# Kernel tuning notes

Measured on AMD Instinct MI355X. Metric: run time of the kernel, lower is better.

## Reference

```python
import jax, jax.numpy as jnp
import numpy as np

V, E, H, M = 256, 512, 512, 128
D = 2 * H  # decoder hidden
B, L_TXT, T_MEL = 32, 256, 800
EPS = 1e-5


def setup_inputs() -> dict:
    key = jax.random.key(0)
    ks = jax.random.split(key, 24)
    s = 0.02
    inp = {
        'x': jax.random.randint(ks[0], (B, L_TXT), 0, V),
        'text_seq_lens': jax.random.randint(ks[1], (B,), 1, L_TXT + 1),
        'y': jax.random.normal(ks[2], (B, T_MEL, M), jnp.float32),
        'mel_spec_lens': jax.random.randint(ks[3], (B,), 1, T_MEL + 1),
        'emb': jax.random.normal(ks[4], (V, E)) * s,
        'conv1_w': jax.random.normal(ks[5], (E, E, 3)) * s,
        'conv1_b': jnp.zeros((E,)),
        'bn1_g': jnp.ones((E,)), 'bn1_b': jnp.zeros((E,)),
        'conv2_w': jax.random.normal(ks[6], (E, E, 3)) * s,
        'conv2_b': jnp.zeros((E,)),
        'bn2_g': jnp.ones((E,)), 'bn2_b': jnp.zeros((E,)),
        'wih_f': jax.random.normal(ks[7], (4 * H, E)) * s,
        'whh_f': jax.random.normal(ks[8], (4 * H, H)) * s,
        'bih_f': jnp.zeros((4 * H,)), 'bhh_f': jnp.zeros((4 * H,)),
        'wih_b': jax.random.normal(ks[9], (4 * H, E)) * s,
        'whh_b': jax.random.normal(ks[10], (4 * H, H)) * s,
        'bih_b': jnp.zeros((4 * H,)), 'bhh_b': jnp.zeros((4 * H,)),
        'dwih': jax.random.normal(ks[11], (4 * D, M)) * s,
        'dwhh': jax.random.normal(ks[12], (4 * D, D)) * s,
        'dbih': jnp.zeros((4 * D,)), 'dbhh': jnp.zeros((4 * D,)),
        'proj_w': jax.random.normal(ks[13], (M, D)) * s,
        'proj_b': jnp.zeros((M,)),
        'gate_w': jax.random.normal(ks[14], (1, D)) * s,
        'gate_b': jnp.zeros((1,)),
    }
    return inp


def _conv_bn_relu(x, w, b, g, beta):
    # x: (B, E, L); training-mode BatchNorm (batch statistics, biased var)
    x = jax.lax.conv_general_dilated(x, w, (1,), [(1, 1)],
                                     dimension_numbers=('NCH', 'OIH', 'NCH')) + b[None, :, None]
    mu = jnp.mean(x, axis=(0, 2), keepdims=True)
    var = jnp.mean((x - mu) ** 2, axis=(0, 2), keepdims=True)
    x = (x - mu) * jax.lax.rsqrt(var + EPS) * g[None, :, None] + beta[None, :, None]
    return jax.nn.relu(x)


def _lstm_last(xseq, lens, wih, whh, bih, bhh):
    # Run LSTM over full padded seq, freezing state past each length.
    # Returns final (h, c) == state at t = len-1 (packed-sequence semantics).
    Bb, T, _ = xseq.shape
    Hh = whh.shape[1]
    pre = jnp.einsum('bte,ge->btg', xseq, wih) + bih + bhh  # (B,T,4H)

    def step(carry, inp):
        h, c = carry
        xt, t = inp
        gates = xt + h @ whh.T
        i, f, g, o = jnp.split(gates, 4, axis=-1)
        c_n = jax.nn.sigmoid(f) * c + jax.nn.sigmoid(i) * jnp.tanh(g)
        h_n = jax.nn.sigmoid(o) * jnp.tanh(c_n)
        valid = (t < lens)[:, None]
        return (jnp.where(valid, h_n, h), jnp.where(valid, c_n, c)), None

    init = (jnp.zeros((Bb, Hh), xseq.dtype), jnp.zeros((Bb, Hh), xseq.dtype))
    (h, c), _ = jax.lax.scan(step, init, (pre.transpose(1, 0, 2), jnp.arange(T)))
    return h, c


def _forward(x, text_seq_lens, y, mel_spec_lens, emb, conv1_w, conv1_b, bn1_g, bn1_b,
             conv2_w, conv2_b, bn2_g, bn2_b, wih_f, whh_f, bih_f, bhh_f,
             wih_b, whh_b, bih_b, bhh_b, dwih, dwhh, dbih, dbhh,
             proj_w, proj_b, gate_w, gate_b):
    xe = emb[x]                       # (B, L, E)
    h = xe.transpose(0, 2, 1)         # (B, E, L)
    h = _conv_bn_relu(h, conv1_w, conv1_b, bn1_g, bn1_b)  # dropout = identity (eval)
    h = _conv_bn_relu(h, conv2_w, conv2_b, bn2_g, bn2_b)
    h = h.transpose(0, 2, 1)          # (B, L, E)

    # bidirectional encoder LSTM final states (packed semantics)
    hf, cf = _lstm_last(h, text_seq_lens, wih_f, whh_f, bih_f, bhh_f)
    # reverse each sequence within its valid length for the backward direction
    t_idx = jnp.arange(h.shape[1])[None, :]
    rev_idx = jnp.clip(text_seq_lens[:, None] - 1 - t_idx, 0, h.shape[1] - 1)
    h_rev = jnp.take_along_axis(h, rev_idx[:, :, None], axis=1)
    hb, cb = _lstm_last(h_rev, text_seq_lens, wih_b, whh_b, bih_b, bhh_b)

    hid = jnp.concatenate([hf, hb], axis=1)  # (B, 2H)
    cel = jnp.concatenate([cf, cb], axis=1)

    Tm = y.shape[1]

    def dec_step(carry, _):
        hd, cd, inp = carry
        gates = inp @ dwih.T + dbih + dbhh + hd @ dwhh.T
        i, f, g, o = jnp.split(gates, 4, axis=-1)
        cd = jax.nn.sigmoid(f) * cd + jax.nn.sigmoid(i) * jnp.tanh(g)
        hd = jax.nn.sigmoid(o) * jnp.tanh(cd)
        mel = hd @ proj_w.T + proj_b          # (B, M)
        gate = hd @ gate_w.T + gate_b         # (B, 1)
        return (hd, cd, mel), (mel, gate[:, 0])

    sos = jnp.zeros((y.shape[0], M), y.dtype)
    _, (mels, gates) = jax.lax.scan(dec_step, (hid, cel, sos), None, length=Tm)
    mel_outputs = mels.transpose(1, 0, 2)     # (B, Tm, M)
    gate_outputs = gates.T                    # (B, Tm)

    mask = jnp.arange(Tm)[None, :] > mel_spec_lens[:, None]  # (B, Tm), strictly >
    masked_mel = jnp.where(mask[:, :, None], 0.0, mel_outputs)
    masked_gate = jnp.where(mask, 1000.0, gate_outputs)
    return masked_mel, masked_gate, mask


def reference(x, text_seq_lens, y, mel_spec_lens, emb, conv1_w, conv1_b, bn1_g, bn1_b,
              conv2_w, conv2_b, bn2_g, bn2_b, wih_f, whh_f, bih_f, bhh_f,
              wih_b, whh_b, bih_b, bhh_b, dwih, dwhh, dbih, dbhh,
              proj_w, proj_b, gate_w, gate_b):
    return _forward(x, text_seq_lens, y, mel_spec_lens, emb, conv1_w, conv1_b,
                    bn1_g, bn1_b, conv2_w, conv2_b, bn2_g, bn2_b,
                    wih_f, whh_f, bih_f, bhh_f, wih_b, whh_b, bih_b, bhh_b,
                    dwih, dwhh, dbih, dbhh, proj_w, proj_b, gate_w, gate_b)
```

## Files before the change

### kernel.cpp

```cpp
#include <hip/hip_runtime.h>


typedef float f4 __attribute__((ext_vector_type(4)));
typedef _Float16 h8 __attribute__((ext_vector_type(8)));
typedef _Float16 half_t;
typedef unsigned long long u64;

#define B_    32
#define LTXT  256
#define TMEL  800
#define EE    512
#define HH    512
#define DD    1024
#define MM    128
#define NROWS 8192
#define GATE_OFF 3276800
#define MASK_OFF 3302400

#define RING_D 801
#define RING_E 257
#define HOP    13

#define WS_MBE        0ull
#define WS_MBD        16384ull
#define WS_HENC       49152ull
#define WS_ZERO_BYTES 81920ull
#define WS_HD         16891904ull
#define WS_BUFX       69386240ull
#define WS_BUFY       77774848ull
#define WS_CONVF      86163456ull
#define WS_WEFF       86163456ull
#define WS_W0         94552064ull
#define WS_WP1        102940672ull
#define WS_WP2        104513536ull
#define WS_WIHP       106086400ull
#define WS_WHHP       110280704ull
#define WS_BSUM       114475008ull
#define WS_BEFF       114491392ull
#define WS_B0         114507776ull
#define WS_MEAN       114524160ull
#define WS_RSTD       114526208ull
#define WS_PROJW      114528256ull
#define WS_PROJG      114790400ull
#define WS_CEL        114823168ull

__device__ __forceinline__ float sigm(float x) { return 1.f / (1.f + __expf(-x)); }
__device__ __forceinline__ float tanh_f(float x) {
    float e = __expf(2.f * x);
    return 1.f - 2.f / (e + 1.f);
}

__device__ __forceinline__ void st_atom64(void* p, u64 v) {
    asm volatile("global_atomic_swap_x2 %0, %1, off" :: "v"(p), "v"(v) : "memory");
}
__device__ __forceinline__ void st_atom32(unsigned* p, unsigned v) {
    asm volatile("global_atomic_swap %0, %1, off" :: "v"(p), "v"(v) : "memory");
}


__global__ void k_embed(const int* __restrict__ x, const float* __restrict__ emb,
                        half_t* __restrict__ out) {
    int row = blockIdx.x;
    int tok = x[row];
    const float* e = emb + (size_t)tok * EE;
    half_t* o = out + (size_t)row * EE;
    for (int c = threadIdx.x; c < EE; c += blockDim.x) o[c] = (half_t)e[c];
}

__global__ void k_packconvw(const float* __restrict__ w, half_t* __restrict__ wp) {
    int idx = blockIdx.x * 256 + threadIdx.x;
    if (idx >= 3 * EE * EE) return;
    int s = idx / (EE * EE);
    int rem = idx - s * EE * EE;
    int eo = rem >> 9, ei = rem & 511;
    wp[idx] = (half_t)w[(size_t)eo * (EE * 3) + ei * 3 + s];
}

__global__ __launch_bounds__(256) void k_conv(const half_t* __restrict__ A,
                                              const half_t* __restrict__ Wp,
                                              const float* __restrict__ bias,
                                              float* __restrict__ out) {
    const int nt = blockIdx.x, et = blockIdx.y;
    const int tid = threadIdx.x;
    const int wv = tid >> 6, l = tid & 63, quad = l >> 4, lo = l & 15;
    const int rowA = nt * 64 + wv * 16 + lo;
    const int eo = et * 16 + lo;
    f4 acc = {0.f, 0.f, 0.f, 0.f};
    for (int s = 0; s < 3; ++s) {
        int lsp = (rowA & 255) + s - 1;
        bool valid = (lsp >= 0) && (lsp < 256);
        int rs = rowA + s - 1;
        rs = rs < 0 ? 0 : (rs > NROWS - 1 ? NROWS - 1 : rs);
        const half_t* ab = A + (size_t)rs * EE;
        const half_t* wb = Wp + ((size_t)s * EE + eo) * EE;
#pragma unroll 4
        for (int ks = 0; ks < 16; ++ks) {
            h8 a = {0, 0, 0, 0, 0, 0, 0, 0};
            if (valid) a = *(const h8*)(ab + ks * 32 + quad * 8);
            h8 b = *(const h8*)(wb + ks * 32 + quad * 8);
            acc = __builtin_amdgcn_mfma_f32_16x16x32_f16(a, b, acc, 0, 0, 0);
        }
    }
    const int orow = nt * 64 + wv * 16 + quad * 4;
    const float bv = bias[eo];
#pragma unroll
    for (int r = 0; r < 4; ++r) out[(size_t)(orow + r) * EE + eo] = acc[r] + bv;
}

__global__ __launch_bounds__(256) void k_bnstats(const float* __restrict__ x,
                                                 float* __restrict__ mean,
                                                 float* __restrict__ rstd) {
    const int c = blockIdx.x;
    float s = 0.f, ss = 0.f;
    for (int n = threadIdx.x; n < NROWS; n += 256) {
        float v = x[(size_t)n * EE + c];
        s += v; ss += v * v;
    }
#pragma unroll
    for (int off = 32; off > 0; off >>= 1) { s += __shfl_down(s, off); ss += __shfl_down(ss, off); }
    __shared__ float as[4], ass[4];
    int wv = threadIdx.x >> 6;
    if ((threadIdx.x & 63) == 0) { as[wv] = s; ass[wv] = ss; }
    __syncthreads();
    if (threadIdx.x == 0) {
        float S = as[0] + as[1] + as[2] + as[3];
        float SS = ass[0] + ass[1] + ass[2] + ass[3];
        float m = S / (float)NROWS;
        float var = SS / (float)NROWS - m * m;
        mean[c] = m;
        rstd[c] = rsqrtf(var + 1e-5f);
    }
}

__global__ void k_bnapply(const float* __restrict__ x, const float* __restrict__ mean,
                          const float* __restrict__ rstd, const float* __restrict__ g,
                          const float* __restrict__ beta, half_t* __restrict__ out) {
    int idx = blockIdx.x * 256 + threadIdx.x;
    if (idx >= NROWS * EE) return;
    int c = idx & (EE - 1);
    float v = (x[idx] - mean[c]) * rstd[c] * g[c] + beta[c];
    out[idx] = (half_t)(v > 0.f ? v : 0.f);
}

__global__ void k_packrec(const float* __restrict__ src, half_t* __restrict__ dst,
                          int Hdim, int kshift, int total) {
    int idx = blockIdx.x * 256 + threadIdx.x;
    if (idx >= total) return;
    int p = idx >> kshift;
    int k = idx & ((1 << kshift) - 1);
    int he = p >> 2, g = p & 3;
    dst[idx] = (half_t)src[((size_t)g * Hdim + he) * (size_t)(1 << kshift) + k];
}

__global__ void k_bsumenc(const float* __restrict__ bf, const float* __restrict__ bhf,
                          const float* __restrict__ bb, const float* __restrict__ bhb,
                          float* __restrict__ bsum) {
    int p = blockIdx.x * 256 + threadIdx.x;
    if (p >= 4096) return;
    int dir = p >> 11, pp = p & 2047;
    int he = pp >> 2, g = pp & 3;
    int row = g * HH + he;
    bsum[p] = dir ? (bb[row] + bhb[row]) : (bf[row] + bhf[row]);
}

__global__ __launch_bounds__(256) void k_weff(const float* __restrict__ dwhh,
                                              const float* __restrict__ dwih,
                                              const float* __restrict__ projw,
                                              half_t* __restrict__ weff,
                                              half_t* __restrict__ w0) {
    int row = blockIdx.x;
    int k = blockIdx.y * 256 + threadIdx.x;
    float v = dwhh[(size_t)row * DD + k];
    float acc = v;
    for (int m = 0; m < MM; ++m) acc += dwih[(size_t)row * MM + m] * projw[(size_t)m * DD + k];
    int p = ((row & (DD - 1)) << 2) | (row >> 10);
    weff[(size_t)p * DD + k] = (half_t)acc;
    w0[(size_t)p * DD + k] = (half_t)v;
}

__global__ void k_bdec(const float* __restrict__ dbih, const float* __restrict__ dbhh,
                       const float* __restrict__ dwih, const float* __restrict__ projb,
                       float* __restrict__ beff, float* __restrict__ b0) {
    int p = blockIdx.x * 256 + threadIdx.x;
    if (p >= 4096) return;
    int he = p >> 2, g = p & 3;
    int row = g * DD + he;
    float bb = dbih[row] + dbhh[row];
    float acc = bb;
    for (int m = 0; m < MM; ++m) acc += dwih[(size_t)row * MM + m] * projb[m];
    b0[p] = bb;
    beff[p] = acc;
}

__global__ void k_cast(const float* __restrict__ src, half_t* __restrict__ dst, int n) {
    int idx = blockIdx.x * 256 + threadIdx.x;
    if (idx < n) dst[idx] = (half_t)src[idx];
}

__global__ void k_projg(const float* __restrict__ gw, half_t* __restrict__ pg) {
    int idx = blockIdx.x * 256 + threadIdx.x;
    if (idx >= 16 * DD) return;
    int row = idx >> 10, k = idx & (DD - 1);
    pg[idx] = (half_t)(row == 0 ? gw[k] : 0.f);
}

__global__ void k_mask(const int* __restrict__ lens, float* __restrict__ out) {
    int idx = blockIdx.x * 256 + threadIdx.x;
    if (idx >= B_ * TMEL) return;
    int b = idx / TMEL, t = idx - b * TMEL;
    out[MASK_OFF + idx] = (t > lens[b]) ? 1.f : 0.f;
}

__global__ __launch_bounds__(512) void k_enc(const half_t* __restrict__ X,
                                             const half_t* __restrict__ wihp,
                                             const half_t* __restrict__ whhp,
                                             const float* __restrict__ bsum,
                                             const int* __restrict__ lens,
                                             half_t* __restrict__ henc,
                                             half_t* __restrict__ hd0,
                                             float* __restrict__ cel,
                                             unsigned* __restrict__ mbE) {
    const int j = blockIdx.x;
    const int dir = j >> 5, sub = j & 31;
    const int tid = threadIdx.x;
    const int wv = tid >> 6, l = tid & 63, quad = l >> 4, lo = l & 15;
    const int rg = wv >> 1, bh = wv & 1;
    const int bfr = bh * 16 + lo;
    const int ue = tid >> 5, ub = tid & 31;

    __shared__ half_t s_hd[32 * 520];
    __shared__ float s_g[32][65];
    __shared__ float s_c[16][32];
    __shared__ float s_h[16][32];
    __shared__ half_t s_hh[16][32];
    __shared__ int s_len[32];

    if (tid < 32) s_len[tid] = lens[tid];
    s_c[ue][ub] = 0.f;
    s_h[ue][ub] = 0.f;

    const int pr = dir * 2048 + sub * 64 + rg * 16 + lo;
    const half_t* wih_b = wihp + (size_t)pr * 512;
    const half_t* whh_b = whhp + (size_t)pr * 512;
    const float bias_n = bsum[pr];

    h8 wihreg[16], whhreg[16];
#pragma unroll
    for (int ks = 0; ks < 16; ++ks) {
        wihreg[ks] = *(const h8*)(wih_b + ks * 32 + quad * 8);
        whhreg[ks] = *(const h8*)(whh_b + ks * 32 + quad * 8);
    }

    int sp = 0, sn = HOP;
    __syncthreads();

    for (int t = 0; t < 256; ++t) {
        if (t > 0) {
            if (tid >= 64 && tid < 96) {
                const unsigned want = (unsigned)t;
                const unsigned* fp = mbE + (size_t)(dir * 32 + sub) * 64 + (tid - 64);
                while (__hip_atomic_load(fp, __ATOMIC_RELAXED, __HIP_MEMORY_SCOPE_AGENT) < want)
                    __builtin_amdgcn_s_sleep(1);
            }
            __syncthreads();
        }

        const half_t* src = henc + (size_t)sp * 32768 + (size_t)dir * 16384;
        h8 tmp0 = *(const h8*)(src + (size_t)(tid + 0 * 512) * 8);
        h8 tmp1 = *(const h8*)(src + (size_t)(tid + 1 * 512) * 8);
        h8 tmp2 = *(const h8*)(src + (size_t)(tid + 2 * 512) * 8);
        h8 tmp3 = *(const h8*)(src + (size_t)(tid + 3 * 512) * 8);

        const int lb = s_len[bfr];
        int tt = (dir == 0) ? t : (lb - 1 - t);
        tt = tt < 0 ? 0 : tt;
        const half_t* xr = X + ((size_t)bfr * 256 + tt) * 512;
        f4 accA = {0.f, 0.f, 0.f, 0.f}, accB = {0.f, 0.f, 0.f, 0.f};
#pragma unroll
        for (int ks = 0; ks < 16; ++ks) {
            h8 a = *(const h8*)(xr + ks * 32 + quad * 8);
            accA = __builtin_amdgcn_mfma_f32_16x16x32_f16(a, wihreg[ks], accA, 0, 0, 0);
        }

        {
            int c0 = tid;
            *(h8*)(s_hd + (size_t)(c0 >> 6) * 520 + (c0 & 63) * 8) = tmp0;
            int c1 = tid + 512;
            *(h8*)(s_hd + (size_t)(c1 >> 6) * 520 + (c1 & 63) * 8) = tmp1;
            int c2 = tid + 1024;
            *(h8*)(s_hd + (size_t)(c2 >> 6) * 520 + (c2 & 63) * 8) = tmp2;
            int c3 = tid + 1536;
            *(h8*)(s_hd + (size_t)(c3 >> 6) * 520 + (c3 & 63) * 8) = tmp3;
        }
        __syncthreads();

#pragma unroll
        for (int ks = 0; ks < 16; ++ks) {
            h8 a = *(const h8*)(s_hd + (size_t)bfr * 520 + ks * 32 + quad * 8);
            accB = __builtin_amdgcn_mfma_f32_16x16x32_f16(a, whhreg[ks], accB, 0, 0, 0);
        }
        const int bm = bh * 16 + quad * 4, cm = rg * 16 + lo;
#pragma unroll
        for (int r = 0; r < 4; ++r) s_g[bm + r][cm] = accA[r] + accB[r] + bias_n;
        __syncthreads();
        {
            float gi = s_g[ub][ue * 4 + 0], gf = s_g[ub][ue * 4 + 1];
            float gg = s_g[ub][ue * 4 + 2], go = s_g[ub][ue * 4 + 3];
            float cn = sigm(gf) * s_c[ue][ub] + sigm(gi) * tanh_f(gg);
            float hn = sigm(go) * tanh_f(cn);
            if (t < s_len[ub]) { s_c[ue][ub] = cn; s_h[ue][ub] = hn; }
            s_hh[ue][ub] = (half_t)s_h[ue][ub];
        }
        __syncthreads();
        if (tid < 64 && t < 255) {
            int b2 = tid >> 1, e8 = (tid & 1) * 8;
            union { half_t h[8]; u64 u[2]; } pk;
#pragma unroll
            for (int i = 0; i < 8; ++i) pk.h[i] = s_hh[e8 + i][b2];
            half_t* dst = henc + (size_t)sn * 32768 + (size_t)dir * 16384
                          + (size_t)b2 * 512 + sub * 16 + e8;
            st_atom64(dst, pk.u[0]);
            st_atom64(dst + 4, pk.u[1]);
            asm volatile("s_waitcnt vmcnt(0)");
            if (tid < 32)
                st_atom32(mbE + ((size_t)(dir * 32 + tid) * 64 + sub), (unsigned)(t + 1));
        }
        if (t < 255) { sp = sn; sn += HOP; if (sn >= RING_E) sn -= RING_E; }
    }
    hd0[(size_t)ub * 1024 + dir * 512 + sub * 16 + ue] = (half_t)s_h[ue][ub];
    cel[(size_t)ub * 1024 + dir * 512 + sub * 16 + ue] = s_c[ue][ub];
}

__global__ __launch_bounds__(512) void k_dec(const half_t* __restrict__ Weff,
                                             const half_t* __restrict__ W0,
                                             const float* __restrict__ beff,
                                             const float* __restrict__ b0,
                                             const half_t* __restrict__ projwb,
                                             const half_t* __restrict__ projg,
                                             const float* __restrict__ projb,
                                             const float* __restrict__ gateb,
                                             const int* __restrict__ mlens,
                                             const float* __restrict__ cel,
                                             half_t* __restrict__ hd,
                                             float* __restrict__ out,
                                             unsigned* __restrict__ mbD) {
    const int j = blockIdx.x;
    const int tid = threadIdx.x;
    const int wv = tid >> 6, l = tid & 63, quad = l >> 4, lo = l & 15;

    __shared__ half_t s_hd[32 * 1032];
    __shared__ float s_g[32][65];
    __shared__ float s_c[16][32];
    __shared__ half_t s_hh[16][32];
    __shared__ int s_len[32];

    if (j < 64) {
        const int rg = wv >> 1, bh = wv & 1;
        const int bfr = bh * 16 + lo;
        const int ue = tid >> 5, ub = tid & 31;

        s_c[ue][ub] = cel[(size_t)ub * 1024 + j * 16 + ue];
        const int pr = j * 64 + rg * 16 + lo;
        const float biasE = beff[pr], bias0 = b0[pr];
        const half_t* wbE = Weff + (size_t)pr * 1024;
        const half_t* wb0 = W0 + (size_t)pr * 1024;

        h8 wreg[32];
#pragma unroll
        for (int ks = 0; ks < 32; ++ks)
            wreg[ks] = *(const h8*)(wbE + ks * 32 + quad * 8);

        int sp = 0, sn = HOP;
        __syncthreads();

        for (int t = 1; t <= TMEL; ++t) {
            if (t > 1) {
                if (tid >= 64 && tid < 128) {
                    const unsigned want = (unsigned)(t - 1);
                    const unsigned* fp = mbD + (size_t)j * 64 + (tid - 64);
                    while (__hip_atomic_load(fp, __ATOMIC_RELAXED, __HIP_MEMORY_SCOPE_AGENT) < want)
                        __builtin_amdgcn_s_sleep(1);
                }
                __syncthreads();
            }

            const half_t* src = hd + (size_t)sp * 32768;
            {
                h8 tp[8];
#pragma unroll
                for (int i = 0; i < 8; ++i)
                    tp[i] = *(const h8*)(src + (size_t)(tid + i * 512) * 8);
#pragma unroll
                for (int i = 0; i < 8; ++i) {
                    int c = tid + i * 512;
                    *(h8*)(s_hd + (size_t)(c >> 7) * 1032 + (c & 127) * 8) = tp[i];
                }
            }
            __syncthreads();

            const half_t* ar = s_hd + (size_t)bfr * 1032 + quad * 8;
            f4 acc = {0.f, 0.f, 0.f, 0.f}, acc2 = {0.f, 0.f, 0.f, 0.f};
            if (t == 1) {
#pragma unroll 8
                for (int ks = 0; ks < 32; ks += 2) {
                    h8 a0 = *(const h8*)(ar + ks * 32);
                    h8 a1 = *(const h8*)(ar + ks * 32 + 32);
                    acc = __builtin_amdgcn_mfma_f32_16x16x32_f16(a0, *(const h8*)(wb0 + ks * 32 + quad * 8), acc, 0, 0, 0);
                    acc2 = __builtin_amdgcn_mfma_f32_16x16x32_f16(a1, *(const h8*)(wb0 + ks * 32 + 32 + quad * 8), acc2, 0, 0, 0);
                }
            } else {
#pragma unroll
                for (int ks = 0; ks < 32; ks += 2) {
                    h8 a0 = *(const h8*)(ar + ks * 32);
                    h8 a1 = *(const h8*)(ar + ks * 32 + 32);
                    acc = __builtin_amdgcn_mfma_f32_16x16x32_f16(a0, wreg[ks], acc, 0, 0, 0);
                    acc2 = __builtin_amdgcn_mfma_f32_16x16x32_f16(a1, wreg[ks + 1], acc2, 0, 0, 0);
                }
            }
            const float bn = (t == 1) ? bias0 : biasE;
            const int bm = bh * 16 + quad * 4, cm = rg * 16 + lo;
#pragma unroll
            for (int r = 0; r < 4; ++r) s_g[bm + r][cm] = acc[r] + acc2[r] + bn;
            __syncthreads();
            {
                float gi = s_g[ub][ue * 4 + 0], gf = s_g[ub][ue * 4 + 1];
                float gg = s_g[ub][ue * 4 + 2], go = s_g[ub][ue * 4 + 3];
                float cn = sigm(gf) * s_c[ue][ub] + sigm(gi) * tanh_f(gg);
                s_c[ue][ub] = cn;
                s_hh[ue][ub] = (half_t)(sigm(go) * tanh_f(cn));
            }
            __syncthreads();
            if (tid < 64) {
                int b2 = tid >> 1, e8 = (tid & 1) * 8;
                union { half_t h[8]; u64 u[2]; } pk;
#pragma unroll
                for (int i = 0; i < 8; ++i) pk.h[i] = s_hh[e8 + i][b2];
                half_t* dst = hd + (size_t)sn * 32768 + (size_t)b2 * 1024 + j * 16 + e8;
                st_atom64(dst, pk.u[0]);
                st_atom64(dst + 4, pk.u[1]);
                asm volatile("s_waitcnt vmcnt(0)");
                st_atom32(mbD + ((size_t)tid * 64 + j), (unsigned)t);
                if (tid < 9)
                    st_atom32(mbD + ((size_t)(64 + tid) * 64 + j), (unsigned)t);
            }
            sp = sn; sn += HOP; if (sn >= RING_D) sn -= RING_D;
        }
    } else {
        const int pj = j - 64;
        const bool meld = (pj < 8);
        const bool duty = (wv < 2);
        const int bh2 = wv & 1;
        const half_t* pw = meld ? (projwb + (size_t)(pj * 16 + lo) * 1024)
                                : (projg + (size_t)lo * 1024);
        const float biasP = meld ? projb[pj * 16 + lo] : gateb[0];

        h8 pwreg[32];
        if (duty) {
#pragma unroll
            for (int ks = 0; ks < 32; ++ks)
                pwreg[ks] = *(const h8*)(pw + ks * 32 + quad * 8);
        }
        if (tid < 32) s_len[tid] = mlens[tid];

        int spP = HOP;
        __syncthreads();

        for (int t = 1; t <= TMEL; ++t) {
            if (tid < 64) {
                const unsigned want = (unsigned)t;
                const unsigned* fp = mbD + (size_t)(64 + pj) * 64 + tid;
                while (__hip_atomic_load(fp, __ATOMIC_RELAXED, __HIP_MEMORY_SCOPE_AGENT) < want)
                    __builtin_amdgcn_s_sleep(1);
            }
            __syncthreads();

            const half_t* src = hd + (size_t)spP * 32768;
            {
                h8 tp[8];
#pragma unroll
                for (int i = 0; i < 8; ++i)
                    tp[i] = *(const h8*)(src + (size_t)(tid + i * 512) * 8);
#pragma unroll
                for (int i = 0; i < 8; ++i) {
                    int c = tid + i * 512;
                    *(h8*)(s_hd + (size_t)(c >> 7) * 1032 + (c & 127) * 8) = tp[i];
                }
            }
            __syncthreads();

            if (duty) {
                const half_t* ar = s_hd + (size_t)(bh2 * 16 + lo) * 1032 + quad * 8;
                f4 accm = {0.f, 0.f, 0.f, 0.f}, accm2 = {0.f, 0.f, 0.f, 0.f};
#pragma unroll
                for (int ks = 0; ks < 32; ks += 2) {
                    h8 a0 = *(const h8*)(ar + ks * 32);
                    h8 a1 = *(const h8*)(ar + ks * 32 + 32);
                    accm = __builtin_amdgcn_mfma_f32_16x16x32_f16(a0, pwreg[ks], accm, 0, 0, 0);
                    accm2 = __builtin_amdgcn_mfma_f32_16x16x32_f16(a1, pwreg[ks + 1], accm2, 0, 0, 0);
                }
                accm[0] += accm2[0]; accm[1] += accm2[1];
                accm[2] += accm2[2]; accm[3] += accm2[3];
                const int pos = t - 1;
                if (meld) {
#pragma unroll
                    for (int r = 0; r < 4; ++r) {
                        int b = bh2 * 16 + quad * 4 + r;
                        float v = accm[r] + biasP;
                        if (pos > s_len[b]) v = 0.f;
                        __builtin_nontemporal_store(v,
                            &out[(size_t)b * (TMEL * MM) + (size_t)pos * MM + pj * 16 + lo]);
                    }
                } else if (lo == 0) {
#pragma unroll
                    for (int r = 0; r < 4; ++r) {
                        int b = bh2 * 16 + quad * 4 + r;
                        float v = accm[r] + biasP;
                        if (pos > s_len[b]) v = 1000.f;
                        __builtin_nontemporal_store(v, &out[GATE_OFF + (size_t)b * TMEL + pos]);
                    }
                }
            }
            __syncthreads();
            spP += HOP; if (spP >= RING_D) spP -= RING_D;
        }
    }
}


extern "C" void kernel_launch(void* const* d_in, const int* in_sizes, int n_in,
                              void* d_out, int out_size, void* d_ws, size_t ws_size,
                              hipStream_t stream) {
    const int* x = (const int*)d_in[0];
    const int* tlens = (const int*)d_in[1];
    const int* mlens = (const int*)d_in[3];
    const float* emb = (const float*)d_in[4];
    const float* c1w = (const float*)d_in[5];
    const float* c1b = (const float*)d_in[6];
    const float* bn1g = (const float*)d_in[7];
    const float* bn1b = (const float*)d_in[8];
    const float* c2w = (const float*)d_in[9];
    const float* c2b = (const float*)d_in[10];
    const float* bn2g = (const float*)d_in[11];
    const float* bn2b = (const float*)d_in[12];
    const float* wihf = (const float*)d_in[13];
    const float* whhf = (const float*)d_in[14];
    const float* bihf = (const float*)d_in[15];
    const float* bhhf = (const float*)d_in[16];
    const float* wihb = (const float*)d_in[17];
    const float* whhb = (const float*)d_in[18];
    const float* bihb = (const float*)d_in[19];
    const float* bhhb = (const float*)d_in[20];
    const float* dwih = (const float*)d_in[21];
    const float* dwhh = (const float*)d_in[22];
    const float* dbih = (const float*)d_in[23];
    const float* dbhh = (const float*)d_in[24];
    const float* projw = (const float*)d_in[25];
    const float* projb = (const float*)d_in[26];
    const float* gatew = (const float*)d_in[27];
    const float* gateb = (const float*)d_in[28];
    float* out = (float*)d_out;
    char* ws = (char*)d_ws;

    unsigned* mbE = (unsigned*)(ws + WS_MBE);
    unsigned* mbD = (unsigned*)(ws + WS_MBD);
    half_t* henc = (half_t*)(ws + WS_HENC);
    half_t* hd = (half_t*)(ws + WS_HD);
    half_t* bufX = (half_t*)(ws + WS_BUFX);
    half_t* bufY = (half_t*)(ws + WS_BUFY);
    float* convf = (float*)(ws + WS_CONVF);
    half_t* weff = (half_t*)(ws + WS_WEFF);
    half_t* w0 = (half_t*)(ws + WS_W0);
    half_t* wp1 = (half_t*)(ws + WS_WP1);
    half_t* wp2 = (half_t*)(ws + WS_WP2);
    float* meanb = (float*)(ws + WS_MEAN);
    float* rstdb = (float*)(ws + WS_RSTD);
    half_t* wihp = (half_t*)(ws + WS_WIHP);
    half_t* whhp = (half_t*)(ws + WS_WHHP);
    float* bsum = (float*)(ws + WS_BSUM);
    float* beff = (float*)(ws + WS_BEFF);
    float* b0 = (float*)(ws + WS_B0);
    half_t* projwb = (half_t*)(ws + WS_PROJW);
    half_t* projg = (half_t*)(ws + WS_PROJG);
    float* cel = (float*)(ws + WS_CEL);

    hipMemsetAsync(d_ws, 0, (size_t)WS_ZERO_BYTES, stream);

    k_embed<<<NROWS, 256, 0, stream>>>(x, emb, bufX);
    k_packconvw<<<(3 * EE * EE + 255) / 256, 256, 0, stream>>>(c1w, wp1);
    k_conv<<<dim3(128, 32), 256, 0, stream>>>(bufX, wp1, c1b, convf);
    k_bnstats<<<EE, 256, 0, stream>>>(convf, meanb, rstdb);
    k_bnapply<<<(NROWS * EE) / 256, 256, 0, stream>>>(convf, meanb, rstdb, bn1g, bn1b, bufY);
    k_packconvw<<<(3 * EE * EE + 255) / 256, 256, 0, stream>>>(c2w, wp2);
    k_conv<<<dim3(128, 32), 256, 0, stream>>>(bufY, wp2, c2b, convf);
    k_bnstats<<<EE, 256, 0, stream>>>(convf, meanb, rstdb);
    k_bnapply<<<(NROWS * EE) / 256, 256, 0, stream>>>(convf, meanb, rstdb, bn2g, bn2b, bufX);

    const int encTot = 2048 * 512;
    k_packrec<<<(encTot + 255) / 256, 256, 0, stream>>>(wihf, wihp, HH, 9, encTot);
    k_packrec<<<(encTot + 255) / 256, 256, 0, stream>>>(wihb, wihp + encTot, HH, 9, encTot);
    k_packrec<<<(encTot + 255) / 256, 256, 0, stream>>>(whhf, whhp, HH, 9, encTot);
    k_packrec<<<(encTot + 255) / 256, 256, 0, stream>>>(whhb, whhp + encTot, HH, 9, encTot);
    k_bsumenc<<<16, 256, 0, stream>>>(bihf, bhhf, bihb, bhhb, bsum);

    k_enc<<<64, 512, 0, stream>>>(bufX, wihp, whhp, bsum, tlens, henc, hd, cel, mbE);

    k_weff<<<dim3(4096, 4), 256, 0, stream>>>(dwhh, dwih, projw, weff, w0);
    k_bdec<<<16, 256, 0, stream>>>(dbih, dbhh, dwih, projb, beff, b0);
    k_cast<<<(MM * DD + 255) / 256, 256, 0, stream>>>(projw, projwb, MM * DD);
    k_projg<<<(16 * DD + 255) / 256, 256, 0, stream>>>(gatew, projg);

    k_dec<<<73, 512, 0, stream>>>(weff, w0, beff, b0, projwb, projg, projb, gateb,
                                  mlens, cel, hd, out, mbD);

    k_mask<<<(B_ * TMEL + 255) / 256, 256, 0, stream>>>(mlens, out);

    (void)in_sizes; (void)n_in; (void)out_size; (void)ws_size;
}
```

Before: 4.901 ms.

## Replace block-wide mailbox wait with per-wave polling of own column slices

Measured after the change: 6.170 ms. 1.26x slower.

```diff
diff --git a/kernel.cpp b/kernel.cpp
--- a/kernel.cpp
+++ b/kernel.cpp
@@ -227,6 +227,7 @@
     const int rg = wv >> 1, bh = wv & 1;
     const int bfr = bh * 16 + lo;
     const int ue = tid >> 5, ub = tid & 31;
+    const int row = l & 31, part = l >> 5;
 
     __shared__ half_t s_hd[32 * 520];
     __shared__ float s_g[32][65];
@@ -255,22 +256,6 @@
     __syncthreads();
 
     for (int t = 0; t < 256; ++t) {
-        if (t > 0) {
-            if (tid >= 64 && tid < 96) {
-                const unsigned want = (unsigned)t;
-                const unsigned* fp = mbE + (size_t)(dir * 32 + sub) * 64 + (tid - 64);
-                while (__hip_atomic_load(fp, __ATOMIC_RELAXED, __HIP_MEMORY_SCOPE_AGENT) < want)
-                    __builtin_amdgcn_s_sleep(1);
-            }
-            __syncthreads();
-        }
-
-        const half_t* src = henc + (size_t)sp * 32768 + (size_t)dir * 16384;
-        h8 tmp0 = *(const h8*)(src + (size_t)(tid + 0 * 512) * 8);
-        h8 tmp1 = *(const h8*)(src + (size_t)(tid + 1 * 512) * 8);
-        h8 tmp2 = *(const h8*)(src + (size_t)(tid + 2 * 512) * 8);
-        h8 tmp3 = *(const h8*)(src + (size_t)(tid + 3 * 512) * 8);
-
         const int lb = s_len[bfr];
         int tt = (dir == 0) ? t : (lb - 1 - t);
         tt = tt < 0 ? 0 : tt;
@@ -282,16 +267,25 @@
             accA = __builtin_amdgcn_mfma_f32_16x16x32_f16(a, wihreg[ks], accA, 0, 0, 0);
         }
 
-        {
-            int c0 = tid;
-            *(h8*)(s_hd + (size_t)(c0 >> 6) * 520 + (c0 & 63) * 8) = tmp0;
-            int c1 = tid + 512;
-            *(h8*)(s_hd + (size_t)(c1 >> 6) * 520 + (c1 & 63) * 8) = tmp1;
-            int c2 = tid + 1024;
-            *(h8*)(s_hd + (size_t)(c2 >> 6) * 520 + (c2 & 63) * 8) = tmp2;
-            int c3 = tid + 1536;
-            *(h8*)(s_hd + (size_t)(c3 >> 6) * 520 + (c3 & 63) * 8) = tmp3;
-        }
+        if (t > 0) {
+            const unsigned want = (unsigned)t;
+            for (;;) {
+                unsigned v = want;
+                if (l < 4)
+                    v = __hip_atomic_load(mbE + (size_t)(dir * 32 + sub) * 64 + wv * 4 + l,
+                                          __ATOMIC_RELAXED, __HIP_MEMORY_SCOPE_AGENT);
+                if (__all(v >= want)) break;
+                __builtin_amdgcn_s_sleep(1);
+            }
+        }
+        const half_t* src = henc + (size_t)sp * 32768 + (size_t)dir * 16384;
+        h8 tp[4];
+#pragma unroll
+        for (int i = 0; i < 4; ++i)
+            tp[i] = *(const h8*)(src + (size_t)row * 512 + (wv * 4 + i) * 16 + part * 8);
+#pragma unroll
+        for (int i = 0; i < 4; ++i)
+            *(h8*)(s_hd + (size_t)row * 520 + (wv * 4 + i) * 16 + part * 8) = tp[i];
         __syncthreads();
 
 #pragma unroll
@@ -347,6 +341,7 @@
     const int j = blockIdx.x;
     const int tid = threadIdx.x;
     const int wv = tid >> 6, l = tid & 63, quad = l >> 4, lo = l & 15;
+    const int row = l & 31, part = l >> 5;
 
     __shared__ half_t s_hd[32 * 1032];
     __shared__ float s_g[32][65];
@@ -375,27 +370,24 @@
 
         for (int t = 1; t <= TMEL; ++t) {
             if (t > 1) {
-                if (tid >= 64 && tid < 128) {
-                    const unsigned want = (unsigned)(t - 1);
-                    const unsigned* fp = mbD + (size_t)j * 64 + (tid - 64);
-                    while (__hip_atomic_load(fp, __ATOMIC_RELAXED, __HIP_MEMORY_SCOPE_AGENT) < want)
-                        __builtin_amdgcn_s_sleep(1);
+                const unsigned want = (unsigned)(t - 1);
+                for (;;) {
+                    unsigned v = want;
+                    if (l < 8)
+                        v = __hip_atomic_load(mbD + (size_t)j * 64 + wv * 8 + l,
+                                              __ATOMIC_RELAXED, __HIP_MEMORY_SCOPE_AGENT);
+                    if (__all(v >= want)) break;
+                    __builtin_amdgcn_s_sleep(1);
                 }
-                __syncthreads();
-            }
-
+            }
             const half_t* src = hd + (size_t)sp * 32768;
-            {
-                h8 tp[8];
-#pragma unroll
-                for (int i = 0; i < 8; ++i)
-                    tp[i] = *(const h8*)(src + (size_t)(tid + i * 512) * 8);
-#pragma unroll
-                for (int i = 0; i < 8; ++i) {
-                    int c = tid + i * 512;
-                    *(h8*)(s_hd + (size_t)(c >> 7) * 1032 + (c & 127) * 8) = tp[i];
-                }
-            }
+            h8 tp[8];
+#pragma unroll
+            for (int i = 0; i < 8; ++i)
+                tp[i] = *(const h8*)(src + (size_t)row * 1024 + (wv * 8 + i) * 16 + part * 8);
+#pragma unroll
+            for (int i = 0; i < 8; ++i)
+                *(h8*)(s_hd + (size_t)row * 1032 + (wv * 8 + i) * 16 + part * 8) = tp[i];
             __syncthreads();
 
             const half_t* ar = s_hd + (size_t)bfr * 1032 + quad * 8;
@@ -466,25 +458,26 @@
         __syncthreads();
 
         for (int t = 1; t <= TMEL; ++t) {
-            if (tid < 64) {
+            {
                 const unsigned want = (unsigned)t;
-                const unsigned* fp = mbD + (size_t)(64 + pj) * 64 + tid;
-                while (__hip_atomic_load(fp, __ATOMIC_RELAXED, __HIP_MEMORY_SCOPE_AGENT) < want)
+                for (;;) {
+                    unsigned v = want;
+                    if (l < 8)
+                        v = __hip_atomic_load(mbD + (size_t)(64 + pj) * 64 + wv * 8 + l,
+                                              __ATOMIC_RELAXED, __HIP_MEMORY_SCOPE_AGENT);
+                    if (__all(v >= want)) break;
                     __builtin_amdgcn_s_sleep(1);
-            }
-            __syncthreads();
-
+                }
+            }
             const half_t* src = hd + (size_t)spP * 32768;
             {
                 h8 tp[8];
 #pragma unroll
                 for (int i = 0; i < 8; ++i)
-                    tp[i] = *(const h8*)(src + (size_t)(tid + i * 512) * 8);
-#pragma unroll
-                for (int i = 0; i < 8; ++i) {
-                    int c = tid + i * 512;
-                    *(h8*)(s_hd + (size_t)(c >> 7) * 1032 + (c & 127) * 8) = tp[i];
-                }
+                    tp[i] = *(const h8*)(src + (size_t)row * 1024 + (wv * 8 + i) * 16 + part * 8);
+#pragma unroll
+                for (int i = 0; i < 8; ++i)
+                    *(h8*)(s_hd + (size_t)row * 1032 + (wv * 8 + i) * 16 + part * 8) = tp[i];
             }
             __syncthreads();
 
```

## Halve persistent recurrent workgroups using 1024-thread blocks to cut cross-block sync

Applied to the files above, without the earlier changes.

After: 11.55 ms. +135.6%, slower.

```diff
diff --git a/kernel.cpp b/kernel.cpp
--- a/kernel.cpp
+++ b/kernel.cpp
@@ -23,26 +23,26 @@
 
 #define WS_MBE        0ull
 #define WS_MBD        16384ull
-#define WS_HENC       49152ull
-#define WS_ZERO_BYTES 81920ull
-#define WS_HD         16891904ull
-#define WS_BUFX       69386240ull
-#define WS_BUFY       77774848ull
-#define WS_CONVF      86163456ull
-#define WS_WEFF       86163456ull
-#define WS_W0         94552064ull
-#define WS_WP1        102940672ull
-#define WS_WP2        104513536ull
-#define WS_WIHP       106086400ull
-#define WS_WHHP       110280704ull
-#define WS_BSUM       114475008ull
-#define WS_BEFF       114491392ull
-#define WS_B0         114507776ull
-#define WS_MEAN       114524160ull
-#define WS_RSTD       114526208ull
-#define WS_PROJW      114528256ull
-#define WS_PROJG      114790400ull
-#define WS_CEL        114823168ull
+#define WS_HENC       32768ull
+#define WS_ZERO_BYTES 98304ull
+#define WS_HD         16875520ull
+#define WS_BUFX       69369856ull
+#define WS_BUFY       77758464ull
+#define WS_CONVF      86147072ull
+#define WS_WEFF       86147072ull
+#define WS_W0         94535680ull
+#define WS_WP1        102924288ull
+#define WS_WP2        104497152ull
+#define WS_WIHP       106070016ull
+#define WS_WHHP       110264320ull
+#define WS_BSUM       114458624ull
+#define WS_BEFF       114475008ull
+#define WS_B0         114491392ull
+#define WS_MEAN       114507776ull
+#define WS_RSTD       114509824ull
+#define WS_PROJW      114511872ull
+#define WS_PROJG      114774016ull
+#define WS_CEL        114806784ull
 
 __device__ __forceinline__ float sigm(float x) { return 1.f / (1.f + __expf(-x)); }
 __device__ __forceinline__ float tanh_f(float x) {
@@ -211,17 +211,17 @@
     out[MASK_OFF + idx] = (t > lens[b]) ? 1.f : 0.f;
 }
 
-__global__ __launch_bounds__(512) void k_enc(const half_t* __restrict__ X,
-                                             const half_t* __restrict__ wihp,
-                                             const half_t* __restrict__ whhp,
-                                             const float* __restrict__ bsum,
-                                             const int* __restrict__ lens,
-                                             half_t* __restrict__ henc,
-                                             half_t* __restrict__ hd0,
-                                             float* __restrict__ cel,
-                                             unsigned* __restrict__ mbE) {
+__global__ __launch_bounds__(1024) void k_enc(const half_t* __restrict__ X,
+                                              const half_t* __restrict__ wihp,
+                                              const half_t* __restrict__ whhp,
+                                              const float* __restrict__ bsum,
+                                              const int* __restrict__ lens,
+                                              half_t* __restrict__ henc,
+                                              half_t* __restrict__ hd0,
+                                              float* __restrict__ cel,
+                                              unsigned* __restrict__ mbE) {
     const int j = blockIdx.x;
-    const int dir = j >> 5, sub = j & 31;
+    const int dir = j >> 4, sub = j & 15;
     const int tid = threadIdx.x;
     const int wv = tid >> 6, l = tid & 63, quad = l >> 4, lo = l & 15;
     const int rg = wv >> 1, bh = wv & 1;
@@ -229,17 +229,17 @@
     const int ue = tid >> 5, ub = tid & 31;
 
     __shared__ half_t s_hd[32 * 520];
-    __shared__ float s_g[32][65];
-    __shared__ float s_c[16][32];
-    __shared__ float s_h[16][32];
-    __shared__ half_t s_hh[16][32];
+    __shared__ float s_g[32][129];
+    __shared__ float s_c[32][32];
+    __shared__ float s_h[32][32];
+    __shared__ half_t s_hh[32][32];
     __shared__ int s_len[32];
 
     if (tid < 32) s_len[tid] = lens[tid];
     s_c[ue][ub] = 0.f;
     s_h[ue][ub] = 0.f;
 
-    const int pr = dir * 2048 + sub * 64 + rg * 16 + lo;
+    const int pr = dir * 2048 + sub * 128 + rg * 16 + lo;
     const half_t* wih_b = wihp + (size_t)pr * 512;
     const half_t* whh_b = whhp + (size_t)pr * 512;
     const float bias_n = bsum[pr];
@@ -255,22 +255,6 @@
     __syncthreads();
 
     for (int t = 0; t < 256; ++t) {
-        if (t > 0) {
-            if (tid >= 64 && tid < 96) {
-                const unsigned want = (unsigned)t;
-                const unsigned* fp = mbE + (size_t)(dir * 32 + sub) * 64 + (tid - 64);
-                while (__hip_atomic_load(fp, __ATOMIC_RELAXED, __HIP_MEMORY_SCOPE_AGENT) < want)
-                    __builtin_amdgcn_s_sleep(1);
-            }
-            __syncthreads();
-        }
-
-        const half_t* src = henc + (size_t)sp * 32768 + (size_t)dir * 16384;
-        h8 tmp0 = *(const h8*)(src + (size_t)(tid + 0 * 512) * 8);
-        h8 tmp1 = *(const h8*)(src + (size_t)(tid + 1 * 512) * 8);
-        h8 tmp2 = *(const h8*)(src + (size_t)(tid + 2 * 512) * 8);
-        h8 tmp3 = *(const h8*)(src + (size_t)(tid + 3 * 512) * 8);
-
         const int lb = s_len[bfr];
         int tt = (dir == 0) ? t : (lb - 1 - t);
         tt = tt < 0 ? 0 : tt;
@@ -282,15 +266,27 @@
             accA = __builtin_amdgcn_mfma_f32_16x16x32_f16(a, wihreg[ks], accA, 0, 0, 0);
         }
 
+        if (t > 0) {
+            if (wv == 1 && l < 16) {
+                const unsigned want = (unsigned)t;
+                const unsigned* fp = mbE + (size_t)(dir * 16 + sub) * 64 + l;
+                while (__hip_atomic_load(fp, __ATOMIC_RELAXED, __HIP_MEMORY_SCOPE_AGENT) < want)
+                    __builtin_amdgcn_s_sleep(1);
+            }
+            __syncthreads();
+        }
+
         {
-            int c0 = tid;
-            *(h8*)(s_hd + (size_t)(c0 >> 6) * 520 + (c0 & 63) * 8) = tmp0;
-            int c1 = tid + 512;
-            *(h8*)(s_hd + (size_t)(c1 >> 6) * 520 + (c1 & 63) * 8) = tmp1;
-            int c2 = tid + 1024;
-            *(h8*)(s_hd + (size_t)(c2 >> 6) * 520 + (c2 & 63) * 8) = tmp2;
-            int c3 = tid + 1536;
-            *(h8*)(s_hd + (size_t)(c3 >> 6) * 520 + (c3 & 63) * 8) = tmp3;
+            const half_t* src = henc + (size_t)sp * 32768 + (size_t)dir * 16384;
+            h8 tp[2];
+#pragma unroll
+            for (int i = 0; i < 2; ++i)
+                tp[i] = *(const h8*)(src + (size_t)(tid + i * 1024) * 8);
+#pragma unroll
+            for (int i = 0; i < 2; ++i) {
+                int c = tid + i * 1024;
+                *(h8*)(s_hd + (size_t)(c >> 6) * 520 + (c & 63) * 8) = tp[i];
+            }
         }
         __syncthreads();
 
@@ -313,54 +309,56 @@
         }
         __syncthreads();
         if (tid < 64 && t < 255) {
-            int b2 = tid >> 1, e8 = (tid & 1) * 8;
-            union { half_t h[8]; u64 u[2]; } pk;
-#pragma unroll
-            for (int i = 0; i < 8; ++i) pk.h[i] = s_hh[e8 + i][b2];
-            half_t* dst = henc + (size_t)sn * 32768 + (size_t)dir * 16384
-                          + (size_t)b2 * 512 + sub * 16 + e8;
-            st_atom64(dst, pk.u[0]);
-            st_atom64(dst + 4, pk.u[1]);
+#pragma unroll
+            for (int i = 0; i < 4; ++i) {
+                int s = i * 64 + tid;
+                int b2 = s >> 3, e8 = (s & 7) * 4;
+                union { half_t h[4]; u64 u; } pk;
+#pragma unroll
+                for (int q = 0; q < 4; ++q) pk.h[q] = s_hh[e8 + q][b2];
+                st_atom64(henc + (size_t)sn * 32768 + (size_t)dir * 16384
+                          + (size_t)b2 * 512 + sub * 32 + e8, pk.u);
+            }
             asm volatile("s_waitcnt vmcnt(0)");
-            if (tid < 32)
-                st_atom32(mbE + ((size_t)(dir * 32 + tid) * 64 + sub), (unsigned)(t + 1));
+            if (tid < 16)
+                st_atom32(mbE + ((size_t)(dir * 16 + tid) * 64 + sub), (unsigned)(t + 1));
         }
         if (t < 255) { sp = sn; sn += HOP; if (sn >= RING_E) sn -= RING_E; }
     }
-    hd0[(size_t)ub * 1024 + dir * 512 + sub * 16 + ue] = (half_t)s_h[ue][ub];
-    cel[(size_t)ub * 1024 + dir * 512 + sub * 16 + ue] = s_c[ue][ub];
-}
-
-__global__ __launch_bounds__(512) void k_dec(const half_t* __restrict__ Weff,
-                                             const half_t* __restrict__ W0,
-                                             const float* __restrict__ beff,
-                                             const float* __restrict__ b0,
-                                             const half_t* __restrict__ projwb,
-                                             const half_t* __restrict__ projg,
-                                             const float* __restrict__ projb,
-                                             const float* __restrict__ gateb,
-                                             const int* __restrict__ mlens,
-                                             const float* __restrict__ cel,
-                                             half_t* __restrict__ hd,
-                                             float* __restrict__ out,
-                                             unsigned* __restrict__ mbD) {
+    hd0[(size_t)ub * 1024 + dir * 512 + sub * 32 + ue] = (half_t)s_h[ue][ub];
+    cel[(size_t)ub * 1024 + dir * 512 + sub * 32 + ue] = s_c[ue][ub];
+}
+
+__global__ __launch_bounds__(1024) void k_dec(const half_t* __restrict__ Weff,
+                                              const half_t* __restrict__ W0,
+                                              const float* __restrict__ beff,
+                                              const float* __restrict__ b0,
+                                              const half_t* __restrict__ projwb,
+                                              const half_t* __restrict__ projg,
+                                              const float* __restrict__ projb,
+                                              const float* __restrict__ gateb,
+                                              const int* __restrict__ mlens,
+                                              const float* __restrict__ cel,
+                                              half_t* __restrict__ hd,
+                                              float* __restrict__ out,
+                                              unsigned* __restrict__ mbD) {
     const int j = blockIdx.x;
     const int tid = threadIdx.x;
     const int wv = tid >> 6, l = tid & 63, quad = l >> 4, lo = l & 15;
+    const int rg = wv >> 1, bh = wv & 1;
+    const int bfr = bh * 16 + lo;
 
     __shared__ half_t s_hd[32 * 1032];
-    __shared__ float s_g[32][65];
-    __shared__ float s_c[16][32];
-    __shared__ half_t s_hh[16][32];
+    __shared__ float s_g[32][129];
+    __shared__ float s_c[32][32];
+    __shared__ half_t s_hh[32][32];
     __shared__ int s_len[32];
 
-    if (j < 64) {
-        const int rg = wv >> 1, bh = wv & 1;
-        const int bfr = bh * 16 + lo;
+    if (j < 32) {
         const int ue = tid >> 5, ub = tid & 31;
 
-        s_c[ue][ub] = cel[(size_t)ub * 1024 + j * 16 + ue];
-        const int pr = j * 64 + rg * 16 + lo;
+        s_c[ue][ub] = cel[(size_t)ub * 1024 + j * 32 + ue];
+        const int pr = j * 128 + rg * 16 + lo;
         const float biasE = beff[pr], bias0 = b0[pr];
         const half_t* wbE = Weff + (size_t)pr * 1024;
         const half_t* wb0 = W0 + (size_t)pr * 1024;
@@ -375,24 +373,24 @@
 
         for (int t = 1; t <= TMEL; ++t) {
             if (t > 1) {
-                if (tid >= 64 && tid < 128) {
+                if (wv == 1 && l < 32) {
                     const unsigned want = (unsigned)(t - 1);
-                    const unsigned* fp = mbD + (size_t)j * 64 + (tid - 64);
+                    const unsigned* fp = mbD + (size_t)j * 64 + l;
                     while (__hip_atomic_load(fp, __ATOMIC_RELAXED, __HIP_MEMORY_SCOPE_AGENT) < want)
                         __builtin_amdgcn_s_sleep(1);
                 }
                 __syncthreads();
             }
 
-            const half_t* src = hd + (size_t)sp * 32768;
             {
-                h8 tp[8];
-#pragma unroll
-                for (int i = 0; i < 8; ++i)
-                    tp[i] = *(const h8*)(src + (size_t)(tid + i * 512) * 8);
-#pragma unroll
-                for (int i = 0; i < 8; ++i) {
-                    int c = tid + i * 512;
+                const half_t* src = hd + (size_t)sp * 32768;
+                h8 tp[4];
+#pragma unroll
+                for (int i = 0; i < 4; ++i)
+                    tp[i] = *(const h8*)(src + (size_t)(tid + i * 1024) * 8);
+#pragma unroll
+                for (int i = 0; i < 4; ++i) {
+                    int c = tid + i * 1024;
                     *(h8*)(s_hd + (size_t)(c >> 7) * 1032 + (c & 127) * 8) = tp[i];
                 }
             }
@@ -431,28 +429,28 @@
             }
             __syncthreads();
             if (tid < 64) {
-                int b2 = tid >> 1, e8 = (tid & 1) * 8;
-                union { half_t h[8]; u64 u[2]; } pk;
-#pragma unroll
-                for (int i = 0; i < 8; ++i) pk.h[i] = s_hh[e8 + i][b2];
-                half_t* dst = hd + (size_t)sn * 32768 + (size_t)b2 * 1024 + j * 16 + e8;
-                st_atom64(dst, pk.u[0]);
-                st_atom64(dst + 4, pk.u[1]);
+#pragma unroll
+                for (int i = 0; i < 4; ++i) {
+                    int s = i * 64 + tid;
+                    int b2 = s >> 3, e8 = (s & 7) * 4;
+                    union { half_t h[4]; u64 u; } pk;
+#pragma unroll
+                    for (int q = 0; q < 4; ++q) pk.h[q] = s_hh[e8 + q][b2];
+                    st_atom64(hd + (size_t)sn * 32768 + (size_t)b2 * 1024 + j * 32 + e8, pk.u);
+                }
                 asm volatile("s_waitcnt vmcnt(0)");
-                st_atom32(mbD + ((size_t)tid * 64 + j), (unsigned)t);
-                if (tid < 9)
-                    st_atom32(mbD + ((size_t)(64 + tid) * 64 + j), (unsigned)t);
+                if (tid < 34)
+                    st_atom32(mbD + ((size_t)tid * 64 + j), (unsigned)t);
             }
             sp = sn; sn += HOP; if (sn >= RING_D) sn -= RING_D;
         }
     } else {
-        const int pj = j - 64;
-        const bool meld = (pj < 8);
-        const bool duty = (wv < 2);
-        const int bh2 = wv & 1;
-        const half_t* pw = meld ? (projwb + (size_t)(pj * 16 + lo) * 1024)
+        const int pj = j - 32;
+        const bool meld = (pj == 0);
+        const bool duty = meld || (wv < 2);
+        const half_t* pw = meld ? (projwb + (size_t)(rg * 16 + lo) * 1024)
                                 : (projg + (size_t)lo * 1024);
-        const float biasP = meld ? projb[pj * 16 + lo] : gateb[0];
+        const float biasP = meld ? projb[rg * 16 + lo] : gateb[0];
 
         h8 pwreg[32];
         if (duty) {
@@ -466,30 +464,30 @@
         __syncthreads();
 
         for (int t = 1; t <= TMEL; ++t) {
-            if (tid < 64) {
+            if (wv == 1 && l < 32) {
                 const unsigned want = (unsigned)t;
-                const unsigned* fp = mbD + (size_t)(64 + pj) * 64 + tid;
+                const unsigned* fp = mbD + (size_t)(32 + pj) * 64 + l;
                 while (__hip_atomic_load(fp, __ATOMIC_RELAXED, __HIP_MEMORY_SCOPE_AGENT) < want)
                     __builtin_amdgcn_s_sleep(1);
             }
             __syncthreads();
 
-            const half_t* src = hd + (size_t)spP * 32768;
             {
-                h8 tp[8];
-#pragma unroll
-                for (int i = 0; i < 8; ++i)
-                    tp[i] = *(const h8*)(src + (size_t)(tid + i * 512) * 8);
-#pragma unroll
-                for (int i = 0; i < 8; ++i) {
-                    int c = tid + i * 512;
+                const half_t* src = hd + (size_t)spP * 32768;
+                h8 tp[4];
+#pragma unroll
+                for (int i = 0; i < 4; ++i)
+                    tp[i] = *(const h8*)(src + (size_t)(tid + i * 1024) * 8);
+#pragma unroll
+                for (int i = 0; i < 4; ++i) {
+                    int c = tid + i * 1024;
                     *(h8*)(s_hd + (size_t)(c >> 7) * 1032 + (c & 127) * 8) = tp[i];
                 }
             }
             __syncthreads();
 
             if (duty) {
-                const half_t* ar = s_hd + (size_t)(bh2 * 16 + lo) * 1032 + quad * 8;
+                const half_t* ar = s_hd + (size_t)bfr * 1032 + quad * 8;
                 f4 accm = {0.f, 0.f, 0.f, 0.f}, accm2 = {0.f, 0.f, 0.f, 0.f};
 #pragma unroll
                 for (int ks = 0; ks < 32; ks += 2) {
@@ -504,16 +502,16 @@
                 if (meld) {
 #pragma unroll
                     for (int r = 0; r < 4; ++r) {
-                        int b = bh2 * 16 + quad * 4 + r;
+                        int b = bh * 16 + quad * 4 + r;
                         float v = accm[r] + biasP;
                         if (pos > s_len[b]) v = 0.f;
                         __builtin_nontemporal_store(v,
-                            &out[(size_t)b * (TMEL * MM) + (size_t)pos * MM + pj * 16 + lo]);
+                            &out[(size_t)b * (TMEL * MM) + (size_t)pos * MM + rg * 16 + lo]);
                     }
                 } else if (lo == 0) {
 #pragma unroll
                     for (int r = 0; r < 4; ++r) {
-                        int b = bh2 * 16 + quad * 4 + r;
+                        int b = bh * 16 + quad * 4 + r;
                         float v = accm[r] + biasP;
                         if (pos > s_len[b]) v = 1000.f;
                         __builtin_nontemporal_store(v, &out[GATE_OFF + (size_t)b * TMEL + pos]);
@@ -602,15 +600,15 @@
     k_packrec<<<(encTot + 255) / 256, 256, 0, stream>>>(whhb, whhp + encTot, HH, 9, encTot);
     k_bsumenc<<<16, 256, 0, stream>>>(bihf, bhhf, bihb, bhhb, bsum);
 
-    k_enc<<<64, 512, 0, stream>>>(bufX, wihp, whhp, bsum, tlens, henc, hd, cel, mbE);
+    k_enc<<<32, 1024, 0, stream>>>(bufX, wihp, whhp, bsum, tlens, henc, hd, cel, mbE);
 
     k_weff<<<dim3(4096, 4), 256, 0, stream>>>(dwhh, dwih, projw, weff, w0);
     k_bdec<<<16, 256, 0, stream>>>(dbih, dbhh, dwih, projb, beff, b0);
     k_cast<<<(MM * DD + 255) / 256, 256, 0, stream>>>(projw, projwb, MM * DD);
     k_projg<<<(16 * DD + 255) / 256, 256, 0, stream>>>(gatew, projg);
 
-    k_dec<<<73, 512, 0, stream>>>(weff, w0, beff, b0, projwb, projg, projb, gateb,
-                                  mlens, cel, hd, out, mbD);
+    k_dec<<<34, 1024, 0, stream>>>(weff, w0, beff, b0, projwb, projg, projb, gateb,
+                                   mlens, cel, hd, out, mbD);
 
     k_mask<<<(B_ * TMEL + 255) / 256, 256, 0, stream>>>(mlens, out);
 
```

## Shrink hidden-state rings to reuse slots and load them with coherent sc0 sc1 loads

Applied to the files above, without the earlier changes.

Result: slower. 5.149 ms (+5.1%).

```diff
diff --git a/kernel.cpp b/kernel.cpp
--- a/kernel.cpp
+++ b/kernel.cpp
@@ -4,6 +4,7 @@
 typedef float f4 __attribute__((ext_vector_type(4)));
 typedef _Float16 h8 __attribute__((ext_vector_type(8)));
 typedef _Float16 half_t;
+typedef unsigned u4 __attribute__((ext_vector_type(4)));
 typedef unsigned long long u64;
 
 #define B_    32
@@ -17,32 +18,32 @@
 #define GATE_OFF 3276800
 #define MASK_OFF 3302400
 
-#define RING_D 801
-#define RING_E 257
+#define RING_D 101
+#define RING_E 33
 #define HOP    13
 
 #define WS_MBE        0ull
 #define WS_MBD        16384ull
 #define WS_HENC       49152ull
-#define WS_ZERO_BYTES 81920ull
-#define WS_HD         16891904ull
-#define WS_BUFX       69386240ull
-#define WS_BUFY       77774848ull
-#define WS_CONVF      86163456ull
-#define WS_WEFF       86163456ull
-#define WS_W0         94552064ull
-#define WS_WP1        102940672ull
-#define WS_WP2        104513536ull
-#define WS_WIHP       106086400ull
-#define WS_WHHP       110280704ull
-#define WS_BSUM       114475008ull
-#define WS_BEFF       114491392ull
-#define WS_B0         114507776ull
-#define WS_MEAN       114524160ull
-#define WS_RSTD       114526208ull
-#define WS_PROJW      114528256ull
-#define WS_PROJG      114790400ull
-#define WS_CEL        114823168ull
+#define WS_ZERO_BYTES 114688ull
+#define WS_HD         2211840ull
+#define WS_BUFX       8830976ull
+#define WS_BUFY       17219584ull
+#define WS_CONVF      25608192ull
+#define WS_WEFF       25608192ull
+#define WS_W0         33996800ull
+#define WS_WP1        42385408ull
+#define WS_WP2        43958272ull
+#define WS_WIHP       45531136ull
+#define WS_WHHP       49725440ull
+#define WS_BSUM       53919744ull
+#define WS_BEFF       53936128ull
+#define WS_B0         53952512ull
+#define WS_MEAN       53968896ull
+#define WS_RSTD       53970944ull
+#define WS_PROJW      53972992ull
+#define WS_PROJG      54235136ull
+#define WS_CEL        54267904ull
 
 __device__ __forceinline__ float sigm(float x) { return 1.f / (1.f + __expf(-x)); }
 __device__ __forceinline__ float tanh_f(float x) {
@@ -55,6 +56,15 @@
 }
 __device__ __forceinline__ void st_atom32(unsigned* p, unsigned v) {
     asm volatile("global_atomic_swap %0, %1, off" :: "v"(p), "v"(v) : "memory");
+}
+__device__ __forceinline__ u4 ld_l3(const void* p) {
+    u4 r;
+    asm volatile("global_load_dwordx4 %0, %1, off sc0 sc1" : "=v"(r) : "v"(p) : "memory");
+    return r;
+}
+__device__ __forceinline__ void wait_vm0() {
+    asm volatile("s_waitcnt vmcnt(0)" ::: "memory");
+    __builtin_amdgcn_sched_barrier(0);
 }
 
 
@@ -266,10 +276,10 @@
         }
 
         const half_t* src = henc + (size_t)sp * 32768 + (size_t)dir * 16384;
-        h8 tmp0 = *(const h8*)(src + (size_t)(tid + 0 * 512) * 8);
-        h8 tmp1 = *(const h8*)(src + (size_t)(tid + 1 * 512) * 8);
-        h8 tmp2 = *(const h8*)(src + (size_t)(tid + 2 * 512) * 8);
-        h8 tmp3 = *(const h8*)(src + (size_t)(tid + 3 * 512) * 8);
+        u4 tmp0 = ld_l3(src + (size_t)(tid + 0 * 512) * 8);
+        u4 tmp1 = ld_l3(src + (size_t)(tid + 1 * 512) * 8);
+        u4 tmp2 = ld_l3(src + (size_t)(tid + 2 * 512) * 8);
+        u4 tmp3 = ld_l3(src + (size_t)(tid + 3 * 512) * 8);
 
         const int lb = s_len[bfr];
         int tt = (dir == 0) ? t : (lb - 1 - t);
@@ -282,15 +292,16 @@
             accA = __builtin_amdgcn_mfma_f32_16x16x32_f16(a, wihreg[ks], accA, 0, 0, 0);
         }
 
+        wait_vm0();
         {
             int c0 = tid;
-            *(h8*)(s_hd + (size_t)(c0 >> 6) * 520 + (c0 & 63) * 8) = tmp0;
+            *(u4*)(s_hd + (size_t)(c0 >> 6) * 520 + (c0 & 63) * 8) = tmp0;
             int c1 = tid + 512;
-            *(h8*)(s_hd + (size_t)(c1 >> 6) * 520 + (c1 & 63) * 8) = tmp1;
+            *(u4*)(s_hd + (size_t)(c1 >> 6) * 520 + (c1 & 63) * 8) = tmp1;
             int c2 = tid + 1024;
-            *(h8*)(s_hd + (size_t)(c2 >> 6) * 520 + (c2 & 63) * 8) = tmp2;
+            *(u4*)(s_hd + (size_t)(c2 >> 6) * 520 + (c2 & 63) * 8) = tmp2;
             int c3 = tid + 1536;
-            *(h8*)(s_hd + (size_t)(c3 >> 6) * 520 + (c3 & 63) * 8) = tmp3;
+            *(u4*)(s_hd + (size_t)(c3 >> 6) * 520 + (c3 & 63) * 8) = tmp3;
         }
         __syncthreads();
 
@@ -384,16 +395,17 @@
                 __syncthreads();
             }
 
-            const half_t* src = hd + (size_t)sp * 32768;
             {
-                h8 tp[8];
+                const half_t* src = hd + (size_t)sp * 32768;
+                u4 tp[8];
 #pragma unroll
                 for (int i = 0; i < 8; ++i)
-                    tp[i] = *(const h8*)(src + (size_t)(tid + i * 512) * 8);
+                    tp[i] = ld_l3(src + (size_t)(tid + i * 512) * 8);
+                wait_vm0();
 #pragma unroll
                 for (int i = 0; i < 8; ++i) {
                     int c = tid + i * 512;
-                    *(h8*)(s_hd + (size_t)(c >> 7) * 1032 + (c & 127) * 8) = tp[i];
+                    *(u4*)(s_hd + (size_t)(c >> 7) * 1032 + (c & 127) * 8) = tp[i];
                 }
             }
             __syncthreads();
@@ -474,16 +486,17 @@
             }
             __syncthreads();
 
-            const half_t* src = hd + (size_t)spP * 32768;
             {
-                h8 tp[8];
+                const half_t* src = hd + (size_t)spP * 32768;
+                u4 tp[8];
 #pragma unroll
                 for (int i = 0; i < 8; ++i)
-                    tp[i] = *(const h8*)(src + (size_t)(tid + i * 512) * 8);
+                    tp[i] = ld_l3(src + (size_t)(tid + i * 512) * 8);
+                wait_vm0();
 #pragma unroll
                 for (int i = 0; i < 8; ++i) {
                     int c = tid + i * 512;
-                    *(h8*)(s_hd + (size_t)(c >> 7) * 1032 + (c & 127) * 8) = tp[i];
+                    *(u4*)(s_hd + (size_t)(c >> 7) * 1032 + (c & 127) * 8) = tp[i];
                 }
             }
             __syncthreads();
```
